# Kernel optimization log

Hardware: AMD Instinct MI355X
Metric: run time of the kernel (lower is better)

## Reference

```python
import jax, jax.numpy as jnp
import numpy as np

B, L, D0, H, K = 16, 256, 64, 128, 512  # batch, seq, feat, hidden, codebook size


def _p(key, shape, scale=0.05):
    return jax.random.normal(key, shape, jnp.float32) * scale


def setup_inputs() -> dict:
    key = jax.random.key(0)
    ks = jax.random.split(key, 32)
    inp = {
        "inputs": jax.random.normal(ks[0], (B, L, D0), jnp.float32),
        "input_lens": jnp.full((B,), L, dtype=jnp.int64),
        "in_mask": jnp.ones((B, L), jnp.float32),
        # encoder params
        "enc_lin1_W": _p(ks[1], (H, D0)), "enc_lin1_b": jnp.zeros((H,), jnp.float32),
        "enc_Wih_f": _p(ks[2], (4 * H, H)), "enc_Whh_f": _p(ks[3], (4 * H, H)), "enc_b_f": jnp.zeros((4 * H,), jnp.float32),
        "enc_Wih_b": _p(ks[4], (4 * H, H)), "enc_Whh_b": _p(ks[5], (4 * H, H)), "enc_b_b": jnp.zeros((4 * H,), jnp.float32),
        "enc_lin2_W": _p(ks[6], (H, 2 * H)), "enc_lin2_b": jnp.zeros((H,), jnp.float32),
        # VQ codebook (K codes of dim H), init uniform(-1/K, 1/K) as in torch
        "vq_emb": jax.random.uniform(ks[7], (K, H), jnp.float32, -1.0 / K, 1.0 / K),
        # decoder params
        "dec_lin1_W": _p(ks[8], (H, D0)), "dec_lin1_b": jnp.zeros((H,), jnp.float32),
        "dec_Wih": _p(ks[9], (4 * H, H)), "dec_Whh": _p(ks[10], (4 * H, H)), "dec_b": jnp.zeros((4 * H,), jnp.float32),
        "attn_Wq": _p(ks[11], (H, H)), "attn_bq": jnp.zeros((H,), jnp.float32),
        "attn_Wk": _p(ks[12], (H, H)), "attn_bk": jnp.zeros((H,), jnp.float32),
        "attn_Wv": _p(ks[13], (H, H)), "attn_bv": jnp.zeros((H,), jnp.float32),
        "dec_lin2_W": _p(ks[14], (D0, H)), "dec_lin2_b": jnp.zeros((D0,), jnp.float32),
    }
    return inp


def _lstm_cell(x, h, c, Wih, Whh, b):
    g = x @ Wih.T + h @ Whh.T + b  # (B, 4H)
    i, f, gg, o = jnp.split(g, 4, axis=-1)
    c = jax.nn.sigmoid(f) * c + jax.nn.sigmoid(i) * jnp.tanh(gg)
    h = jax.nn.sigmoid(o) * jnp.tanh(c)
    return h, c


def _lstm_scan(x_blh, Wih, Whh, b, reverse=False):
    Bb = x_blh.shape[0]
    Hh = Whh.shape[1]
    init = (jnp.zeros((Bb, Hh), x_blh.dtype), jnp.zeros((Bb, Hh), x_blh.dtype))

    def step(carry, x):
        h, c = _lstm_cell(x, carry[0], carry[1], Wih, Whh, b)
        return (h, c), h

    _, hs = jax.lax.scan(step, init, jnp.swapaxes(x_blh, 0, 1), reverse=reverse)
    return jnp.swapaxes(hs, 0, 1)  # (B, L, H)


def _forward(inputs, in_mask, p):
    # ---- encoder: Linear -> ReLU -> BiLSTM -> Linear (full-length sequences) ----
    enc_x = jax.nn.relu(inputs @ p["enc_lin1_W"].T + p["enc_lin1_b"])
    hf = _lstm_scan(enc_x, p["enc_Wih_f"], p["enc_Whh_f"], p["enc_b_f"], reverse=False)
    hb = _lstm_scan(enc_x, p["enc_Wih_b"], p["enc_Whh_b"], p["enc_b_b"], reverse=True)
    ze = jnp.concatenate([hf, hb], axis=-1) @ p["enc_lin2_W"].T + p["enc_lin2_b"]  # (B,L,H)

    # ---- VQ: nearest codebook entry (expanded ||a-b||^2, avoids (B,L,K,C) tensor) ----
    emb = p["vq_emb"]  # (K, H)
    dist = (jnp.sum(ze * ze, -1, keepdims=True)
            - 2.0 * jnp.einsum("blc,kc->blk", ze, emb)
            + jnp.sum(emb * emb, -1)[None, None, :])  # (B,L,K)
    nearest = jnp.argmin(dist, axis=-1)  # (B,L) int
    zq = emb[nearest]  # (B,L,H)
    dec_in = ze + jax.lax.stop_gradient(zq - ze)  # straight-through

    k_proj = dec_in @ p["attn_Wk"].T + p["attn_bk"]  # (B,L,H)
    v_proj = dec_in @ p["attn_Wv"].T + p["attn_bv"]
    scale = 1.0 / jnp.sqrt(jnp.float32(H))
    mask_add = jnp.where(in_mask == 0, -1e9, 0.0).astype(jnp.float32)  # (B,L)

    def dec_step(carry, _):
        h, c, tok = carry
        x = jax.nn.relu(tok @ p["dec_lin1_W"].T + p["dec_lin1_b"])  # (B,H)
        h, c = _lstm_cell(x, h, c, p["dec_Wih"], p["dec_Whh"], p["dec_b"])
        q = h @ p["attn_Wq"].T + p["attn_bq"]  # (B,H)
        scores = jnp.einsum("bd,bld->bl", q, k_proj) * scale + mask_add
        attn = jax.nn.softmax(scores, axis=-1)  # (B,L)
        ctx = jnp.einsum("bl,bld->bd", attn, v_proj)  # (B,H)
        out = ctx @ p["dec_lin2_W"].T + p["dec_lin2_b"]  # (B,D0)
        return (h, c, out), (out, attn)

    Bb = inputs.shape[0]
    init = (jnp.zeros((Bb, H), jnp.float32), jnp.zeros((Bb, H), jnp.float32), jnp.zeros((Bb, D0), jnp.float32))
    _, (outs, attns) = jax.lax.scan(dec_step, init, None, length=dec_in.shape[1])
    dec_out = jnp.swapaxes(outs, 0, 1)  # (B,L,D0)
    attn_w = jnp.swapaxes(attns, 0, 1)  # (B,L,L)
    return dec_out, attn_w, ze, zq


def reference(inputs, input_lens, in_mask, enc_lin1_W, enc_lin1_b, enc_Wih_f, enc_Whh_f, enc_b_f,
              enc_Wih_b, enc_Whh_b, enc_b_b, enc_lin2_W, enc_lin2_b, vq_emb,
              dec_lin1_W, dec_lin1_b, dec_Wih, dec_Whh, dec_b,
              attn_Wq, attn_bq, attn_Wk, attn_bk, attn_Wv, attn_bv, dec_lin2_W, dec_lin2_b):
    p = dict(enc_lin1_W=enc_lin1_W, enc_lin1_b=enc_lin1_b, enc_Wih_f=enc_Wih_f, enc_Whh_f=enc_Whh_f,
             enc_b_f=enc_b_f, enc_Wih_b=enc_Wih_b, enc_Whh_b=enc_Whh_b, enc_b_b=enc_b_b,
             enc_lin2_W=enc_lin2_W, enc_lin2_b=enc_lin2_b, vq_emb=vq_emb,
             dec_lin1_W=dec_lin1_W, dec_lin1_b=dec_lin1_b, dec_Wih=dec_Wih, dec_Whh=dec_Whh, dec_b=dec_b,
             attn_Wq=attn_Wq, attn_bq=attn_bq, attn_Wk=attn_Wk, attn_bk=attn_bk,
             attn_Wv=attn_Wv, attn_bv=attn_bv, dec_lin2_W=dec_lin2_W, dec_lin2_b=dec_lin2_b)
    return _forward(inputs, in_mask, p)
```

## Files before the change

kernel.cpp:

```cpp
#include <hip/hip_runtime.h>

#define Bn  16
#define Ln  256
#define D0n 64
#define Hn  128
#define H4n 512
#define Kn  512
#define BLn 4096

typedef float f4 __attribute__((ext_vector_type(4)));
typedef unsigned long long u64;

__device__ __forceinline__ float sigf(float x) { return 1.0f / (1.0f + expf(-x)); }

__device__ __forceinline__ float fma4v(f4 w, f4 x, float acc) {
    acc = fmaf(w.x, x.x, acc);
    acc = fmaf(w.y, x.y, acc);
    acc = fmaf(w.z, x.z, acc);
    acc = fmaf(w.w, x.w, acc);
    return acc;
}

__device__ __forceinline__ float dotn(const f4* __restrict__ a,
                                      const f4* __restrict__ w, int n4) {
    float a0 = 0.f, a1 = 0.f, a2 = 0.f, a3 = 0.f;
    for (int i = 0; i < n4; i += 4) {
        a0 = fma4v(a[i], w[i], a0);
        a1 = fma4v(a[i + 1], w[i + 1], a1);
        a2 = fma4v(a[i + 2], w[i + 2], a2);
        a3 = fma4v(a[i + 3], w[i + 3], a3);
    }
    return (a0 + a1) + (a2 + a3);
}

__device__ __forceinline__ void tag_store(u64* p, float v, unsigned tag) {
    u64 pk = ((u64)tag << 32) | (u64)__float_as_uint(v);
    __hip_atomic_store(p, pk, __ATOMIC_RELAXED, __HIP_MEMORY_SCOPE_AGENT);
}
__device__ __forceinline__ float tag_poll(u64* p, unsigned tag) {
    u64 v;
    do {
        v = __hip_atomic_load(p, __ATOMIC_RELAXED, __HIP_MEMORY_SCOPE_AGENT);
    } while ((unsigned)(v >> 32) != tag);
    return __uint_as_float((unsigned)v);
}

__global__ __launch_bounds__(256)
void k_gemm(const float* __restrict__ X, const float* __restrict__ W,
            const float* __restrict__ b, float* __restrict__ Y,
            int K, int out_dim, int do_relu, float scale) {
    __shared__ float wtT[16384];
    const int K4 = K >> 2;
    const int tid = threadIdx.x;
    const int c = tid & 63, rpart = tid >> 6;
    const f4* W4 = (const f4*)W;
    const int per = K4 >> 2;
    for (int j = 0; j < per; ++j) {
        int col = rpart * per + j;
        f4 v = W4[(size_t)(blockIdx.x * 64 + c) * K4 + col];
        wtT[(col * 4 + 0) * 64 + c] = v.x;
        wtT[(col * 4 + 1) * 64 + c] = v.y;
        wtT[(col * 4 + 2) * 64 + c] = v.z;
        wtT[(col * 4 + 3) * 64 + c] = v.w;
    }
    __syncthreads();
    const f4* X4 = (const f4*)X;
    const float bc = b ? b[blockIdx.x * 64 + c] : 0.f;
    for (int i = 0; i < 16; ++i) {
        int r = blockIdx.y * 64 + i * 4 + rpart;
        const f4* xr = X4 + (size_t)r * K4;
        float a0 = 0.f, a1 = 0.f, a2 = 0.f, a3 = 0.f;
        for (int k4 = 0; k4 < K4; ++k4) {
            f4 xv = xr[k4];
            a0 = fmaf(xv.x, wtT[(k4 * 4 + 0) * 64 + c], a0);
            a1 = fmaf(xv.y, wtT[(k4 * 4 + 1) * 64 + c], a1);
            a2 = fmaf(xv.z, wtT[(k4 * 4 + 2) * 64 + c], a2);
            a3 = fmaf(xv.w, wtT[(k4 * 4 + 3) * 64 + c], a3);
        }
        float acc = scale * ((a0 + a1) + (a2 + a3)) + bc;
        if (do_relu) acc = fmaxf(acc, 0.f);
        Y[(size_t)r * out_dim + blockIdx.x * 64 + c] = acc;
    }
}

__global__ void k_prep(const float* __restrict__ attn_Wq, float* __restrict__ WqT,
                       const f4* __restrict__ dec_Wih, f4* __restrict__ WihL,
                       const f4* __restrict__ whf, const f4* __restrict__ whb,
                       f4* __restrict__ WhhL, int* __restrict__ zbuf) {
    const int blk = blockIdx.x, tid = threadIdx.x;
    if (blk < 64) {
        int idx = blk * 256 + tid;
        int c = idx >> 7, r = idx & 127;
        WqT[idx] = attn_Wq[(size_t)r * Hn + c];
    } else if (blk < 128) {
        int idx = (blk - 64) * 256 + tid;
        int t = idx & 511, side = (idx >> 9) & 1, k = idx >> 10;
        int rl = t >> 1;
        int grow = (rl >> 6) * 128 + side * 64 + (rl & 63);
        WihL[idx] = dec_Wih[(size_t)grow * 32 + (t & 1) * 16 + k];
    } else if (blk < 192) {
        int idx = (blk - 128) * 256 + tid;
        int row = idx & 511, k = (idx >> 9) & 15, dir = idx >> 13;
        const f4* src = dir ? whb : whf;
        WhhL[idx] = src[(size_t)row * 32 + 16 + k];
    } else {
        int idx = (blk - 192) * 256 + tid;
        if (idx < 8192) zbuf[idx] = 0;
    }
}

__global__ void k_rearrKQF(const f4* __restrict__ in, f4* __restrict__ out) {
    int idx = blockIdx.x * blockDim.x + threadIdx.x;
    if (idx >= 131072) return;
    int tid = idx & 511, k = (idx >> 9) & 15, b = idx >> 13;
    out[idx] = in[((size_t)b * 256 + (tid >> 1)) * 32 + (tid & 1) * 16 + k];
}

__global__ void k_cst(const float* __restrict__ kp, const float* __restrict__ bq,
                      const float* __restrict__ mask, float* __restrict__ cst) {
    int p = blockIdx.x * blockDim.x + threadIdx.x;
    if (p >= BLn) return;
    float a = dotn((const f4*)bq, (const f4*)(kp + (size_t)p * Hn), Hn >> 2);
    cst[p] = a * 0.088388347648318447f + (mask[p] == 0.f ? -1e9f : 0.f);
}

__global__ void k_codenorm(const float* __restrict__ emb, float* __restrict__ c2) {
    int k = blockIdx.x * blockDim.x + threadIdx.x;
    if (k >= Kn) return;
    const f4* e4 = (const f4*)(emb + (size_t)k * Hn);
    float acc = 0.f;
    for (int i = 0; i < Hn / 4; ++i) {
        f4 v = e4[i];
        acc = fmaf(v.x, v.x, acc); acc = fmaf(v.y, v.y, acc);
        acc = fmaf(v.z, v.z, acc); acc = fmaf(v.w, v.w, acc);
    }
    c2[k] = acc;
}

__global__ __launch_bounds__(128)
void k_vqpick(const float* __restrict__ dist, const float* __restrict__ emb,
              float* __restrict__ zq) {
    const int p = blockIdx.x, tid = threadIdx.x;
    __shared__ int best_s;
    if (tid < 64) {
        float best = 3.0e38f; int bi = 0;
        for (int j = 0; j < 8; ++j) {
            int k = j * 64 + tid;
            float d = dist[(size_t)p * Kn + k];
            if (d < best) { best = d; bi = k; }
        }
        for (int off = 32; off > 0; off >>= 1) {
            float ov = __shfl_xor(best, off);
            int   oi = __shfl_xor(bi, off);
            if (ov < best || (ov == best && oi < bi)) { best = ov; bi = oi; }
        }
        if (tid == 0) best_s = bi;
    }
    __syncthreads();
    zq[(size_t)p * Hn + tid] = emb[(size_t)best_s * Hn + tid];
}

__global__ __launch_bounds__(512, 1)
void k_lstm3(const float* __restrict__ xWf, const float* __restrict__ xWb,
             const float* __restrict__ Whh_f, const float* __restrict__ Whh_b,
             const float* __restrict__ WhhL_g, float* __restrict__ hcat) {
    const int b   = blockIdx.x & 15;
    const int dir = blockIdx.x >> 4;
    const int tid = threadIdx.x;
    const float* xW  = dir ? xWb : xWf;
    const f4* Whh4   = (const f4*)(dir ? Whh_b : Whh_f);

    __shared__ __align__(16) f4 wh2_s[16 * 512];
    __shared__ __align__(16) float h_s[Hn];
    __shared__ float g_s[H4n];

    f4 w[16];
#pragma unroll
    for (int f = 0; f < 16; ++f) w[f] = Whh4[(size_t)tid * 32 + f];
#pragma unroll
    for (int f = 0; f < 16; ++f) asm volatile("" : "+v"(w[f]));

    const f4* WhhL4 = (const f4*)WhhL_g;
#pragma unroll
    for (int k = 0; k < 16; ++k)
        wh2_s[k * 512 + tid] = WhhL4[(size_t)dir * 8192 + k * 512 + tid];

    float c_reg = 0.f;
    if (tid < Hn) h_s[tid] = 0.f;

    const int t0 = dir ? (Ln - 1) : 0;
    float xw_v = xW[((size_t)b * Ln + t0) * H4n + tid];
    __syncthreads();

    for (int s = 0; s < Ln; ++s) {
        const int t = dir ? (Ln - 1 - s) : s;
        float xw_n = 0.f;
        if (s + 1 < Ln) {
            int tn = dir ? (Ln - 2 - s) : (s + 1);
            xw_n = xW[((size_t)b * Ln + tn) * H4n + tid];
        }
        {
            const f4* h4 = (const f4*)h_s;
            float a0 = 0.f, a1 = 0.f, a2 = 0.f, a3 = 0.f;
#pragma unroll
            for (int f = 0; f < 16; f += 4) {
                a0 = fma4v(w[f],     h4[f],     a0);
                a1 = fma4v(w[f + 1], h4[f + 1], a1);
                a2 = fma4v(w[f + 2], h4[f + 2], a2);
                a3 = fma4v(w[f + 3], h4[f + 3], a3);
            }
#pragma unroll
            for (int f = 0; f < 16; f += 4) {
                a0 = fma4v(wh2_s[f * 512 + tid],       h4[16 + f],     a0);
                a1 = fma4v(wh2_s[(f + 1) * 512 + tid], h4[16 + f + 1], a1);
                a2 = fma4v(wh2_s[(f + 2) * 512 + tid], h4[16 + f + 2], a2);
                a3 = fma4v(wh2_s[(f + 3) * 512 + tid], h4[16 + f + 3], a3);
            }
            g_s[tid] = (a0 + a1) + (a2 + a3) + xw_v;
        }
        __syncthreads();
        if (tid < Hn) {
            float ig = sigf(g_s[tid]);
            float fg = sigf(g_s[Hn + tid]);
            float gg = tanhf(g_s[2 * Hn + tid]);
            float og = sigf(g_s[3 * Hn + tid]);
            c_reg = fg * c_reg + ig * gg;
            float hv = og * tanhf(c_reg);
            h_s[tid] = hv;
            hcat[((size_t)b * Ln + t) * (2 * Hn) + dir * Hn + tid] = hv;
        }
        __syncthreads();
        xw_v = xw_n;
    }
}

__global__ __launch_bounds__(512, 1)
void k_decoder(const float* __restrict__ kqF_g, const float* __restrict__ vw_g,
               const float* __restrict__ cst_g,
               const float* __restrict__ W1,  const float* __restrict__ b1_g,
               const float* __restrict__ WihL_g, const float* __restrict__ Whh,
               const float* __restrict__ bd_g, u64* gxd,
               float* __restrict__ dec_out, float* __restrict__ attn_w) {
    const int b    = blockIdx.x & 15;
    const int side = blockIdx.x >> 4;
    const int tid  = threadIdx.x;

    __shared__ __align__(16) f4 wih_s[16 * 512];
    __shared__ __align__(16) float tok_s[D0n];
    __shared__ __align__(16) float x_s[Hn];
    __shared__ __align__(16) float h_s[Hn];
    __shared__ float g_loc[256];
    __shared__ float s_s[Ln];
    __shared__ float attn_sp[8][33];
    __shared__ float cst_s[Ln];
    __shared__ float b1_s[Hn];

    const int rl = tid >> 1, ghalf = tid & 1;
    const int grow = (rl >> 6) * 128 + side * 64 + (rl & 63);

    const f4* Whh4 = (const f4*)Whh;
    f4 whh[16];
#pragma unroll
    for (int f = 0; f < 16; ++f) whh[f] = Whh4[(size_t)grow * 32 + ghalf * 16 + f];
    float bdr = bd_g[grow];
    const int o = tid >> 3, slab = tid & 7;
    float vwr[32];
#pragma unroll
    for (int l = 0; l < 32; ++l)
        vwr[l] = vw_g[((size_t)b * Ln + slab * 32 + l) * D0n + o];
#pragma unroll
    for (int f = 0; f < 16; ++f) asm volatile("" : "+v"(whh[f]));
#pragma unroll
    for (int l = 0; l < 32; ++l) asm volatile("" : "+v"(vwr[l]));
    asm volatile("" : "+v"(bdr));

    const f4* WihL4 = (const f4*)WihL_g;
#pragma unroll
    for (int k = 0; k < 16; ++k)
        wih_s[k * 512 + tid] = WihL4[(size_t)k * 1024 + side * 512 + tid];
    if (tid < D0n) tok_s[tid] = 0.f;
    if (tid < Hn)  { h_s[tid] = 0.f; b1_s[tid] = b1_g[tid]; }
    if (tid < Ln)  cst_s[tid] = cst_g[(size_t)b * Ln + tid];
    float c_reg = 0.f;
    __syncthreads();

    u64* gx_mine = gxd + (b * 2 + side) * 128;
    u64* gx_peer = gxd + (b * 2 + (side ^ 1)) * 128;

    const int ar = tid >> 2, ap = tid & 3;
    const f4* W1_4 = (const f4*)W1;
    const f4* kqF  = (const f4*)kqF_g + (size_t)b * 8192;
    const int dbase = (tid & 1) * 16;

    for (int t = 0; t < Ln; ++t) {
        {
            const f4* t4 = (const f4*)tok_s;
            float u0 = 0.f, u1 = 0.f;
#pragma unroll
            for (int k = 0; k < 4; k += 2) {
                f4 wa  = W1_4[(size_t)ar * 16 + ap * 4 + k];
                f4 wb2 = W1_4[(size_t)ar * 16 + ap * 4 + k + 1];
                u0 = fma4v(wa,  t4[ap * 4 + k],     u0);
                u1 = fma4v(wb2, t4[ap * 4 + k + 1], u1);
            }
            float a = u0 + u1;
            a += __shfl_xor(a, 1);
            a += __shfl_xor(a, 2);
            if (ap == 0) x_s[ar] = fmaxf(a + b1_s[ar], 0.f);
        }
        __syncthreads();
        {
            const f4* x4 = (const f4*)x_s + ghalf * 16;
            const f4* h4 = (const f4*)h_s + ghalf * 16;
            float a0 = 0.f, a1 = 0.f, a2 = 0.f, a3 = 0.f;
#pragma unroll
            for (int f = 0; f < 16; f += 4) {
                a0 = fma4v(wih_s[f * 512 + tid],       x4[f],     a0);
                a1 = fma4v(wih_s[(f + 1) * 512 + tid], x4[f + 1], a1);
                a2 = fma4v(wih_s[(f + 2) * 512 + tid], x4[f + 2], a2);
                a3 = fma4v(wih_s[(f + 3) * 512 + tid], x4[f + 3], a3);
            }
#pragma unroll
            for (int f = 0; f < 16; f += 4) {
                a0 = fma4v(whh[f],     h4[f],     a0);
                a1 = fma4v(whh[f + 1], h4[f + 1], a1);
                a2 = fma4v(whh[f + 2], h4[f + 2], a2);
                a3 = fma4v(whh[f + 3], h4[f + 3], a3);
            }
            float a = (a0 + a1) + (a2 + a3);
            a += __shfl_xor(a, 1);
            if (ghalf == 0) g_loc[rl] = a + bdr;
        }
        __syncthreads();
        if (tid < 64) {
            float ig = sigf(g_loc[tid]);
            float fg = sigf(g_loc[64 + tid]);
            float gg = tanhf(g_loc[128 + tid]);
            float og = sigf(g_loc[192 + tid]);
            c_reg = fg * c_reg + ig * gg;
            float hv = og * tanhf(c_reg);
            h_s[side * 64 + tid] = hv;
            tag_store(&gx_mine[(t & 1) * 64 + tid], hv, (unsigned)(t + 1));
            h_s[(side ^ 1) * 64 + tid] =
                tag_poll(&gx_peer[(t & 1) * 64 + tid], (unsigned)(t + 1));
        }
        __syncthreads();
        {
            const f4* h4 = (const f4*)h_s;
            float a0 = 0.f, a1 = 0.f;
#pragma unroll
            for (int k = 0; k < 16; k += 2) {
                f4 q0 = kqF[(size_t)k * 512 + tid];
                f4 q1 = kqF[(size_t)(k + 1) * 512 + tid];
                a0 = fma4v(q0, h4[dbase + k],     a0);
                a1 = fma4v(q1, h4[dbase + k + 1], a1);
            }
            float a = a0 + a1;
            a += __shfl_xor(a, 1);
            if ((tid & 1) == 0) s_s[tid >> 1] = a + cst_s[tid >> 1];
        }
        __syncthreads();
        if (tid < 64) {
            float v0 = s_s[tid],       v1 = s_s[tid + 64];
            float v2 = s_s[tid + 128], v3 = s_s[tid + 192];
            float m = fmaxf(fmaxf(v0, v1), fmaxf(v2, v3));
#pragma unroll
            for (int o2 = 32; o2 > 0; o2 >>= 1) m = fmaxf(m, __shfl_xor(m, o2));
            float e0 = expf(v0 - m), e1 = expf(v1 - m);
            float e2 = expf(v2 - m), e3 = expf(v3 - m);
            float ss = (e0 + e1) + (e2 + e3);
#pragma unroll
            for (int o2 = 32; o2 > 0; o2 >>= 1) ss += __shfl_xor(ss, o2);
            float inv = 1.f / ss;
            e0 *= inv; e1 *= inv; e2 *= inv; e3 *= inv;
            attn_sp[tid >> 5][tid & 31] = e0;
            attn_sp[(tid + 64) >> 5][tid & 31] = e1;
            attn_sp[(tid + 128) >> 5][tid & 31] = e2;
            attn_sp[(tid + 192) >> 5][tid & 31] = e3;
            if (side == 0) {
                float* aw = attn_w + ((size_t)b * Ln + t) * Ln;
                aw[tid] = e0; aw[tid + 64] = e1;
                aw[tid + 128] = e2; aw[tid + 192] = e3;
            }
        }
        __syncthreads();
        {
            const float* as = attn_sp[slab];
            float g0 = 0.f, g1 = 0.f, g2 = 0.f, g3 = 0.f;
#pragma unroll
            for (int l = 0; l < 32; l += 4) {
                g0 = fmaf(as[l],     vwr[l],     g0);
                g1 = fmaf(as[l + 1], vwr[l + 1], g1);
                g2 = fmaf(as[l + 2], vwr[l + 2], g2);
                g3 = fmaf(as[l + 3], vwr[l + 3], g3);
            }
            float a = (g0 + g1) + (g2 + g3);
            a += __shfl_xor(a, 1);
            a += __shfl_xor(a, 2);
            a += __shfl_xor(a, 4);
            if (slab == 0) {
                tok_s[o] = a;
                if (side == 1) dec_out[((size_t)b * Ln + t) * D0n + o] = a;
            }
        }
        __syncthreads();
    }
}

extern "C" void kernel_launch(void* const* d_in, const int* in_sizes, int n_in,
                              void* d_out, int out_size, void* d_ws, size_t ws_size,
                              hipStream_t stream) {
    const float* inputs     = (const float*)d_in[0];
    const float* in_mask    = (const float*)d_in[2];
    const float* enc_lin1_W = (const float*)d_in[3];
    const float* enc_lin1_b = (const float*)d_in[4];
    const float* enc_Wih_f  = (const float*)d_in[5];
    const float* enc_Whh_f  = (const float*)d_in[6];
    const float* enc_b_f    = (const float*)d_in[7];
    const float* enc_Wih_b  = (const float*)d_in[8];
    const float* enc_Whh_b  = (const float*)d_in[9];
    const float* enc_b_b    = (const float*)d_in[10];
    const float* enc_lin2_W = (const float*)d_in[11];
    const float* enc_lin2_b = (const float*)d_in[12];
    const float* vq_emb     = (const float*)d_in[13];
    const float* dec_lin1_W = (const float*)d_in[14];
    const float* dec_lin1_b = (const float*)d_in[15];
    const float* dec_Wih    = (const float*)d_in[16];
    const float* dec_Whh    = (const float*)d_in[17];
    const float* dec_b      = (const float*)d_in[18];
    const float* attn_Wq    = (const float*)d_in[19];
    const float* attn_bq    = (const float*)d_in[20];
    const float* attn_Wk    = (const float*)d_in[21];
    const float* attn_bk    = (const float*)d_in[22];
    const float* attn_Wv    = (const float*)d_in[23];
    const float* attn_bv    = (const float*)d_in[24];
    const float* dec_lin2_W = (const float*)d_in[25];
    const float* dec_lin2_b = (const float*)d_in[26];

    float* out     = (float*)d_out;
    float* dec_out = out;
    float* attn_w  = out + 262144;
    float* ze      = out + 1310720;
    float* zq      = out + 1835008;

    float* ws    = (float*)d_ws;
    float* enc_x = ws;
    float* xWf   = enc_x + 524288;
    float* xWb   = xWf + 2097152;
    float* hcat  = xWb + 2097152;
    float* kp    = hcat + 1048576;
    float* vp    = kp + 524288;
    float* c2    = vp + 524288;
    u64*   gxd   = (u64*)(c2 + 512);
    float* WqT   = enc_x;
    float* WihL  = enc_x + 16384;
    float* WhhL  = enc_x + 16384 + 65536;
    float* dist  = xWf;
    float* KQF   = xWf;
    float* kq    = xWb;
    float* vw    = xWb + 524288;
    float* cst   = xWb + 786432;

    dim3 blk(256);
    k_gemm<<<dim3(2, 64), blk, 0, stream>>>(inputs, enc_lin1_W, enc_lin1_b, enc_x, D0n, Hn, 1, 1.f);
    k_gemm<<<dim3(8, 64), blk, 0, stream>>>(enc_x, enc_Wih_f, enc_b_f, xWf, Hn, H4n, 0, 1.f);
    k_gemm<<<dim3(8, 64), blk, 0, stream>>>(enc_x, enc_Wih_b, enc_b_b, xWb, Hn, H4n, 0, 1.f);
    k_prep<<<224, 256, 0, stream>>>(attn_Wq, WqT, (const f4*)dec_Wih, (f4*)WihL,
                                    (const f4*)enc_Whh_f, (const f4*)enc_Whh_b,
                                    (f4*)WhhL, (int*)gxd);
    k_lstm3<<<32, 512, 0, stream>>>(xWf, xWb, enc_Whh_f, enc_Whh_b, WhhL, hcat);
    k_gemm<<<dim3(2, 64), blk, 0, stream>>>(hcat, enc_lin2_W, enc_lin2_b, ze, 2 * Hn, Hn, 0, 1.f);
    k_codenorm<<<2, 256, 0, stream>>>(vq_emb, c2);
    k_gemm<<<dim3(8, 64), blk, 0, stream>>>(ze, vq_emb, c2, dist, Hn, Kn, 0, -2.f);
    k_vqpick<<<BLn, 128, 0, stream>>>(dist, vq_emb, zq);
    k_gemm<<<dim3(2, 64), blk, 0, stream>>>(zq, attn_Wk, attn_bk, kp, Hn, Hn, 0, 1.f);
    k_gemm<<<dim3(2, 64), blk, 0, stream>>>(zq, attn_Wv, attn_bv, vp, Hn, Hn, 0, 1.f);
    k_gemm<<<dim3(2, 64), blk, 0, stream>>>(kp, WqT, nullptr, kq, Hn, Hn, 0, 0.088388347648318447f);
    k_rearrKQF<<<512, 256, 0, stream>>>((const f4*)kq, (f4*)KQF);
    k_gemm<<<dim3(1, 64), blk, 0, stream>>>(vp, dec_lin2_W, dec_lin2_b, vw, Hn, D0n, 0, 1.f);
    k_cst<<<Bn, 256, 0, stream>>>(kp, attn_bq, in_mask, cst);
    k_decoder<<<32, 512, 0, stream>>>(KQF, vw, cst,
                                      dec_lin1_W, dec_lin1_b,
                                      WihL, dec_Whh, dec_b, gxd,
                                      dec_out, attn_w);
}
```

Baseline: 1.644 ms.

## Split decoder across four cooperating blocks per batch with distributed softmax

The sequential decoder moves from two 512-thread blocks per batch element to four 256-thread blocks. Each block owns a quarter of the LSTM gate rows and a 64-position slice of the attention keys, and the key-query and lin1 weights are now staged in shared memory. Softmax is computed per slice, and the partial max, sum and value-weighted outputs are exchanged through tagged global flags, then merged online. This spreads the per-step work over more compute units and takes global loads off the critical loop. In exchange, every timestep now needs two rounds of cross-block polling among four peers instead of one round with a single peer.

```diff
diff --git a/kernel.cpp b/kernel.cpp
--- a/kernel.cpp
+++ b/kernel.cpp
@@ -86,7 +86,9 @@
 __global__ void k_prep(const float* __restrict__ attn_Wq, float* __restrict__ WqT,
                        const f4* __restrict__ dec_Wih, f4* __restrict__ WihL,
                        const f4* __restrict__ whf, const f4* __restrict__ whb,
-                       f4* __restrict__ WhhL, int* __restrict__ zbuf) {
+                       f4* __restrict__ WhhL,
+                       const f4* __restrict__ dec_W1, f4* __restrict__ w1L,
+                       int* __restrict__ zbuf, int zcount) {
     const int blk = blockIdx.x, tid = threadIdx.x;
     if (blk < 64) {
         int idx = blk * 256 + tid;
@@ -94,26 +96,31 @@
         WqT[idx] = attn_Wq[(size_t)r * Hn + c];
     } else if (blk < 128) {
         int idx = (blk - 64) * 256 + tid;
-        int t = idx & 511, side = (idx >> 9) & 1, k = idx >> 10;
+        int t = idx & 255, k = (idx >> 8) & 15, s = idx >> 12;
         int rl = t >> 1;
-        int grow = (rl >> 6) * 128 + side * 64 + (rl & 63);
+        int grow = (rl >> 5) * 128 + s * 32 + (rl & 31);
         WihL[idx] = dec_Wih[(size_t)grow * 32 + (t & 1) * 16 + k];
     } else if (blk < 192) {
         int idx = (blk - 128) * 256 + tid;
         int row = idx & 511, k = (idx >> 9) & 15, dir = idx >> 13;
         const f4* src = dir ? whb : whf;
         WhhL[idx] = src[(size_t)row * 32 + 16 + k];
+    } else if (blk < 200) {
+        int idx = (blk - 192) * 256 + tid;
+        int t = idx & 255, k = idx >> 8;
+        w1L[idx] = dec_W1[((size_t)(t >> 1)) * 16 + (t & 1) * 8 + k];
     } else {
-        int idx = (blk - 192) * 256 + tid;
-        if (idx < 8192) zbuf[idx] = 0;
-    }
-}
-
-__global__ void k_rearrKQF(const f4* __restrict__ in, f4* __restrict__ out) {
+        int idx = (blk - 200) * 256 + tid;
+        if (idx < zcount) zbuf[idx] = 0;
+    }
+}
+
+__global__ void k_rearrKQL(const f4* __restrict__ in, f4* __restrict__ out) {
     int idx = blockIdx.x * blockDim.x + threadIdx.x;
     if (idx >= 131072) return;
-    int tid = idx & 511, k = (idx >> 9) & 15, b = idx >> 13;
-    out[idx] = in[((size_t)b * 256 + (tid >> 1)) * 32 + (tid & 1) * 16 + k];
+    int tid = idx & 255, k = (idx >> 8) & 7, bs = idx >> 11;
+    int row = (bs >> 2) * 256 + (bs & 3) * 64 + (tid >> 2);
+    out[idx] = in[(size_t)row * 32 + (tid & 3) * 8 + k];
 }
 
 __global__ void k_cst(const float* __restrict__ kp, const float* __restrict__ bq,
@@ -234,79 +241,86 @@
     }
 }
 
-__global__ __launch_bounds__(512, 1)
-void k_decoder(const float* __restrict__ kqF_g, const float* __restrict__ vw_g,
+__global__ __launch_bounds__(256, 1)
+void k_decoder(const float* __restrict__ kqL_g, const float* __restrict__ vw_g,
                const float* __restrict__ cst_g,
-               const float* __restrict__ W1,  const float* __restrict__ b1_g,
+               const float* __restrict__ w1L_g, const float* __restrict__ b1_g,
                const float* __restrict__ WihL_g, const float* __restrict__ Whh,
-               const float* __restrict__ bd_g, u64* gxd,
+               const float* __restrict__ bd_g,
+               u64* gxh, u64* gxp,
                float* __restrict__ dec_out, float* __restrict__ attn_w) {
-    const int b    = blockIdx.x & 15;
-    const int side = blockIdx.x >> 4;
-    const int tid  = threadIdx.x;
-
-    __shared__ __align__(16) f4 wih_s[16 * 512];
+    const int b   = blockIdx.x & 15;
+    const int s   = blockIdx.x >> 4;
+    const int tid = threadIdx.x;
+
+    __shared__ __align__(16) f4 wih_s[4096];
+    __shared__ __align__(16) f4 kq_s[2048];
+    __shared__ __align__(16) f4 w1_s[2048];
     __shared__ __align__(16) float tok_s[D0n];
     __shared__ __align__(16) float x_s[Hn];
     __shared__ __align__(16) float h_s[Hn];
-    __shared__ float g_loc[256];
-    __shared__ float s_s[Ln];
-    __shared__ float attn_sp[8][33];
-    __shared__ float cst_s[Ln];
+    __shared__ float g_loc[Hn];
+    __shared__ float s_loc[64];
+    __shared__ float pP[4][72];
+    __shared__ float peermz[8];
+    __shared__ float cst_s[64];
     __shared__ float b1_s[Hn];
 
     const int rl = tid >> 1, ghalf = tid & 1;
-    const int grow = (rl >> 6) * 128 + side * 64 + (rl & 63);
+    const int grow = (rl >> 5) * 128 + s * 32 + (rl & 31);
+    const int wavep = tid >> 6, lane = tid & 63;
 
     const f4* Whh4 = (const f4*)Whh;
     f4 whh[16];
 #pragma unroll
     for (int f = 0; f < 16; ++f) whh[f] = Whh4[(size_t)grow * 32 + ghalf * 16 + f];
     float bdr = bd_g[grow];
-    const int o = tid >> 3, slab = tid & 7;
-    float vwr[32];
-#pragma unroll
-    for (int l = 0; l < 32; ++l)
-        vwr[l] = vw_g[((size_t)b * Ln + slab * 32 + l) * D0n + o];
+    float vwr[16];
+#pragma unroll
+    for (int k = 0; k < 16; ++k)
+        vwr[k] = vw_g[((size_t)b * Ln + s * 64 + wavep * 16 + k) * D0n + lane];
 #pragma unroll
     for (int f = 0; f < 16; ++f) asm volatile("" : "+v"(whh[f]));
 #pragma unroll
-    for (int l = 0; l < 32; ++l) asm volatile("" : "+v"(vwr[l]));
+    for (int k = 0; k < 16; ++k) asm volatile("" : "+v"(vwr[k]));
     asm volatile("" : "+v"(bdr));
 
     const f4* WihL4 = (const f4*)WihL_g;
 #pragma unroll
     for (int k = 0; k < 16; ++k)
-        wih_s[k * 512 + tid] = WihL4[(size_t)k * 1024 + side * 512 + tid];
+        wih_s[k * 256 + tid] = WihL4[(size_t)s * 4096 + k * 256 + tid];
+    const f4* kqL4 = (const f4*)kqL_g;
+#pragma unroll
+    for (int k = 0; k < 8; ++k)
+        kq_s[k * 256 + tid] = kqL4[(size_t)(b * 4 + s) * 2048 + k * 256 + tid];
+    const f4* w1L4 = (const f4*)w1L_g;
+#pragma unroll
+    for (int k = 0; k < 8; ++k)
+        w1_s[k * 256 + tid] = w1L4[k * 256 + tid];
     if (tid < D0n) tok_s[tid] = 0.f;
     if (tid < Hn)  { h_s[tid] = 0.f; b1_s[tid] = b1_g[tid]; }
-    if (tid < Ln)  cst_s[tid] = cst_g[(size_t)b * Ln + tid];
+    if (tid < 64)  cst_s[tid] = cst_g[(size_t)b * Ln + s * 64 + tid];
     float c_reg = 0.f;
     __syncthreads();
 
-    u64* gx_mine = gxd + (b * 2 + side) * 128;
-    u64* gx_peer = gxd + (b * 2 + (side ^ 1)) * 128;
-
-    const int ar = tid >> 2, ap = tid & 3;
-    const f4* W1_4 = (const f4*)W1;
-    const f4* kqF  = (const f4*)kqF_g + (size_t)b * 8192;
-    const int dbase = (tid & 1) * 16;
+    u64* gxh_mine = gxh + (size_t)((b * 4 + s) * 2) * 32;
+    u64* gxp_mine = gxp + (size_t)((b * 4 + s) * 2) * 66;
+    const int sp1 = (s + 1) & 3, sp2 = (s + 2) & 3, sp3 = (s + 3) & 3;
 
     for (int t = 0; t < Ln; ++t) {
+        const unsigned tg = (unsigned)(t + 1);
+        const int par = t & 1;
         {
             const f4* t4 = (const f4*)tok_s;
             float u0 = 0.f, u1 = 0.f;
 #pragma unroll
-            for (int k = 0; k < 4; k += 2) {
-                f4 wa  = W1_4[(size_t)ar * 16 + ap * 4 + k];
-                f4 wb2 = W1_4[(size_t)ar * 16 + ap * 4 + k + 1];
-                u0 = fma4v(wa,  t4[ap * 4 + k],     u0);
-                u1 = fma4v(wb2, t4[ap * 4 + k + 1], u1);
+            for (int k = 0; k < 8; k += 2) {
+                u0 = fma4v(w1_s[k * 256 + tid],       t4[ghalf * 8 + k],     u0);
+                u1 = fma4v(w1_s[(k + 1) * 256 + tid], t4[ghalf * 8 + k + 1], u1);
             }
             float a = u0 + u1;
             a += __shfl_xor(a, 1);
-            a += __shfl_xor(a, 2);
-            if (ap == 0) x_s[ar] = fmaxf(a + b1_s[ar], 0.f);
+            if (ghalf == 0) x_s[rl] = fmaxf(a + b1_s[rl], 0.f);
         }
         __syncthreads();
         {
@@ -315,10 +329,10 @@
             float a0 = 0.f, a1 = 0.f, a2 = 0.f, a3 = 0.f;
 #pragma unroll
             for (int f = 0; f < 16; f += 4) {
-                a0 = fma4v(wih_s[f * 512 + tid],       x4[f],     a0);
-                a1 = fma4v(wih_s[(f + 1) * 512 + tid], x4[f + 1], a1);
-                a2 = fma4v(wih_s[(f + 2) * 512 + tid], x4[f + 2], a2);
-                a3 = fma4v(wih_s[(f + 3) * 512 + tid], x4[f + 3], a3);
+                a0 = fma4v(wih_s[f * 256 + tid],       x4[f],     a0);
+                a1 = fma4v(wih_s[(f + 1) * 256 + tid], x4[f + 1], a1);
+                a2 = fma4v(wih_s[(f + 2) * 256 + tid], x4[f + 2], a2);
+                a3 = fma4v(wih_s[(f + 3) * 256 + tid], x4[f + 3], a3);
             }
 #pragma unroll
             for (int f = 0; f < 16; f += 4) {
@@ -332,76 +346,85 @@
             if (ghalf == 0) g_loc[rl] = a + bdr;
         }
         __syncthreads();
-        if (tid < 64) {
+        if (tid < 32) {
             float ig = sigf(g_loc[tid]);
-            float fg = sigf(g_loc[64 + tid]);
-            float gg = tanhf(g_loc[128 + tid]);
-            float og = sigf(g_loc[192 + tid]);
+            float fg = sigf(g_loc[32 + tid]);
+            float gg = tanhf(g_loc[64 + tid]);
+            float og = sigf(g_loc[96 + tid]);
             c_reg = fg * c_reg + ig * gg;
             float hv = og * tanhf(c_reg);
-            h_s[side * 64 + tid] = hv;
-            tag_store(&gx_mine[(t & 1) * 64 + tid], hv, (unsigned)(t + 1));
-            h_s[(side ^ 1) * 64 + tid] =
-                tag_poll(&gx_peer[(t & 1) * 64 + tid], (unsigned)(t + 1));
+            h_s[s * 32 + tid] = hv;
+            tag_store(&gxh_mine[par * 32 + tid], hv, tg);
+            h_s[sp1 * 32 + tid] = tag_poll(
+                gxh + (size_t)((b * 4 + sp1) * 2 + par) * 32 + tid, tg);
+            h_s[sp2 * 32 + tid] = tag_poll(
+                gxh + (size_t)((b * 4 + sp2) * 2 + par) * 32 + tid, tg);
+            h_s[sp3 * 32 + tid] = tag_poll(
+                gxh + (size_t)((b * 4 + sp3) * 2 + par) * 32 + tid, tg);
         }
         __syncthreads();
         {
+            const int ll = tid >> 2, dp = tid & 3;
             const f4* h4 = (const f4*)h_s;
-            float a0 = 0.f, a1 = 0.f;
-#pragma unroll
-            for (int k = 0; k < 16; k += 2) {
-                f4 q0 = kqF[(size_t)k * 512 + tid];
-                f4 q1 = kqF[(size_t)(k + 1) * 512 + tid];
-                a0 = fma4v(q0, h4[dbase + k],     a0);
-                a1 = fma4v(q1, h4[dbase + k + 1], a1);
+            float u0 = 0.f, u1 = 0.f;
+#pragma unroll
+            for (int k = 0; k < 8; k += 2) {
+                u0 = fma4v(kq_s[k * 256 + tid],       h4[dp * 8 + k],     u0);
+                u1 = fma4v(kq_s[(k + 1) * 256 + tid], h4[dp * 8 + k + 1], u1);
             }
-            float a = a0 + a1;
-            a += __shfl_xor(a, 1);
-            if ((tid & 1) == 0) s_s[tid >> 1] = a + cst_s[tid >> 1];
-        }
-        __syncthreads();
-        if (tid < 64) {
-            float v0 = s_s[tid],       v1 = s_s[tid + 64];
-            float v2 = s_s[tid + 128], v3 = s_s[tid + 192];
-            float m = fmaxf(fmaxf(v0, v1), fmaxf(v2, v3));
-#pragma unroll
-            for (int o2 = 32; o2 > 0; o2 >>= 1) m = fmaxf(m, __shfl_xor(m, o2));
-            float e0 = expf(v0 - m), e1 = expf(v1 - m);
-            float e2 = expf(v2 - m), e3 = expf(v3 - m);
-            float ss = (e0 + e1) + (e2 + e3);
-#pragma unroll
-            for (int o2 = 32; o2 > 0; o2 >>= 1) ss += __shfl_xor(ss, o2);
-            float inv = 1.f / ss;
-            e0 *= inv; e1 *= inv; e2 *= inv; e3 *= inv;
-            attn_sp[tid >> 5][tid & 31] = e0;
-            attn_sp[(tid + 64) >> 5][tid & 31] = e1;
-            attn_sp[(tid + 128) >> 5][tid & 31] = e2;
-            attn_sp[(tid + 192) >> 5][tid & 31] = e3;
-            if (side == 0) {
-                float* aw = attn_w + ((size_t)b * Ln + t) * Ln;
-                aw[tid] = e0; aw[tid + 64] = e1;
-                aw[tid + 128] = e2; aw[tid + 192] = e3;
-            }
-        }
-        __syncthreads();
-        {
-            const float* as = attn_sp[slab];
-            float g0 = 0.f, g1 = 0.f, g2 = 0.f, g3 = 0.f;
-#pragma unroll
-            for (int l = 0; l < 32; l += 4) {
-                g0 = fmaf(as[l],     vwr[l],     g0);
-                g1 = fmaf(as[l + 1], vwr[l + 1], g1);
-                g2 = fmaf(as[l + 2], vwr[l + 2], g2);
-                g3 = fmaf(as[l + 3], vwr[l + 3], g3);
-            }
-            float a = (g0 + g1) + (g2 + g3);
+            float a = u0 + u1;
             a += __shfl_xor(a, 1);
             a += __shfl_xor(a, 2);
-            a += __shfl_xor(a, 4);
-            if (slab == 0) {
-                tok_s[o] = a;
-                if (side == 1) dec_out[((size_t)b * Ln + t) * D0n + o] = a;
-            }
+            if (dp == 0) s_loc[ll] = a + cst_s[ll];
+        }
+        __syncthreads();
+        float e, m_own, Z_own;
+        {
+            float v = s_loc[lane];
+            float m = v;
+#pragma unroll
+            for (int o2 = 32; o2 > 0; o2 >>= 1) m = fmaxf(m, __shfl_xor(m, o2));
+            e = expf(v - m);
+            float Z = e;
+#pragma unroll
+            for (int o2 = 32; o2 > 0; o2 >>= 1) Z += __shfl_xor(Z, o2);
+            m_own = m; Z_own = Z;
+            float acc = 0.f;
+#pragma unroll
+            for (int k = 0; k < 16; ++k)
+                acc = fmaf(__shfl(e, wavep * 16 + k), vwr[k], acc);
+            pP[wavep][lane] = acc;
+        }
+        __syncthreads();
+        float Pown = 0.f, p1 = 0.f, p2 = 0.f, p3 = 0.f;
+        if (tid < 64) {
+            Pown = pP[0][tid] + pP[1][tid] + pP[2][tid] + pP[3][tid];
+            tag_store(&gxp_mine[par * 66 + tid], Pown, tg);
+            p1 = tag_poll(gxp + (size_t)((b * 4 + sp1) * 2 + par) * 66 + tid, tg);
+            p2 = tag_poll(gxp + (size_t)((b * 4 + sp2) * 2 + par) * 66 + tid, tg);
+            p3 = tag_poll(gxp + (size_t)((b * 4 + sp3) * 2 + par) * 66 + tid, tg);
+        } else if (tid < 70) {
+            int idx = tid - 64;
+            if (idx == 0) tag_store(&gxp_mine[par * 66 + 64], m_own, tg);
+            if (idx == 1) tag_store(&gxp_mine[par * 66 + 65], Z_own, tg);
+            int spi = idx >> 1, which = idx & 1;
+            int sp = (s + 1 + spi) & 3;
+            peermz[idx] = tag_poll(
+                gxp + (size_t)((b * 4 + sp) * 2 + par) * 66 + 64 + which, tg);
+        }
+        __syncthreads();
+        if (tid < 64) {
+            float m1 = peermz[0], Z1 = peermz[1];
+            float m2 = peermz[2], Z2 = peermz[3];
+            float m3 = peermz[4], Z3 = peermz[5];
+            float M = fmaxf(fmaxf(m_own, m1), fmaxf(m2, m3));
+            float w0 = expf(m_own - M), w1 = expf(m1 - M);
+            float w2 = expf(m2 - M), w3 = expf(m3 - M);
+            float inv = 1.f / (w0 * Z_own + w1 * Z1 + w2 * Z2 + w3 * Z3);
+            float ov = (w0 * Pown + w1 * p1 + w2 * p2 + w3 * p3) * inv;
+            tok_s[tid] = ov;
+            if (s == 0) dec_out[((size_t)b * Ln + t) * D0n + tid] = ov;
+            attn_w[((size_t)b * Ln + t) * Ln + s * 64 + tid] = e * w0 * inv;
         }
         __syncthreads();
     }
@@ -451,12 +474,14 @@
     float* kp    = hcat + 1048576;
     float* vp    = kp + 524288;
     float* c2    = vp + 524288;
-    u64*   gxd   = (u64*)(c2 + 512);
+    u64*   gxh   = (u64*)(c2 + 512);
+    u64*   gxp   = gxh + 4096;
     float* WqT   = enc_x;
     float* WihL  = enc_x + 16384;
     float* WhhL  = enc_x + 16384 + 65536;
+    float* w1L   = enc_x + 16384 + 2 * 65536;
     float* dist  = xWf;
-    float* KQF   = xWf;
+    float* KQL   = xWf;
     float* kq    = xWb;
     float* vw    = xWb + 524288;
     float* cst   = xWb + 786432;
@@ -465,9 +490,10 @@
     k_gemm<<<dim3(2, 64), blk, 0, stream>>>(inputs, enc_lin1_W, enc_lin1_b, enc_x, D0n, Hn, 1, 1.f);
     k_gemm<<<dim3(8, 64), blk, 0, stream>>>(enc_x, enc_Wih_f, enc_b_f, xWf, Hn, H4n, 0, 1.f);
     k_gemm<<<dim3(8, 64), blk, 0, stream>>>(enc_x, enc_Wih_b, enc_b_b, xWb, Hn, H4n, 0, 1.f);
-    k_prep<<<224, 256, 0, stream>>>(attn_Wq, WqT, (const f4*)dec_Wih, (f4*)WihL,
+    k_prep<<<298, 256, 0, stream>>>(attn_Wq, WqT, (const f4*)dec_Wih, (f4*)WihL,
                                     (const f4*)enc_Whh_f, (const f4*)enc_Whh_b,
-                                    (f4*)WhhL, (int*)gxd);
+                                    (f4*)WhhL, (const f4*)dec_lin1_W, (f4*)w1L,
+                                    (int*)gxh, 25088);
     k_lstm3<<<32, 512, 0, stream>>>(xWf, xWb, enc_Whh_f, enc_Whh_b, WhhL, hcat);
     k_gemm<<<dim3(2, 64), blk, 0, stream>>>(hcat, enc_lin2_W, enc_lin2_b, ze, 2 * Hn, Hn, 0, 1.f);
     k_codenorm<<<2, 256, 0, stream>>>(vq_emb, c2);
@@ -476,11 +502,12 @@
     k_gemm<<<dim3(2, 64), blk, 0, stream>>>(zq, attn_Wk, attn_bk, kp, Hn, Hn, 0, 1.f);
     k_gemm<<<dim3(2, 64), blk, 0, stream>>>(zq, attn_Wv, attn_bv, vp, Hn, Hn, 0, 1.f);
     k_gemm<<<dim3(2, 64), blk, 0, stream>>>(kp, WqT, nullptr, kq, Hn, Hn, 0, 0.088388347648318447f);
-    k_rearrKQF<<<512, 256, 0, stream>>>((const f4*)kq, (f4*)KQF);
+    k_rearrKQL<<<512, 256, 0, stream>>>((const f4*)kq, (f4*)KQL);
     k_gemm<<<dim3(1, 64), blk, 0, stream>>>(vp, dec_lin2_W, dec_lin2_b, vw, Hn, D0n, 0, 1.f);
     k_cst<<<Bn, 256, 0, stream>>>(kp, attn_bq, in_mask, cst);
-    k_decoder<<<32, 512, 0, stream>>>(KQF, vw, cst,
-                                      dec_lin1_W, dec_lin1_b,
-                                      WihL, dec_Whh, dec_b, gxd,
+    k_decoder<<<64, 256, 0, stream>>>(KQL, vw, cst,
+                                      w1L, dec_lin1_b,
+                                      WihL, dec_Whh, dec_b,
+                                      gxh, gxp,
                                       dec_out, attn_w);
 }
```

Measured after the change: 1.795 ms. 1.09x slower.
